# Performance work log

Hardware: AMD Instinct MI355X
Metric: run time of the kernel (lower is better)

The kernel has to match this reference:

```python
import jax, jax.numpy as jnp
import numpy as np

NUM_OBJ = 3
MIN_OBJ_SCALE = 0.1
MAX_OBJ_SCALE = 0.8
MIN_Y_SCALE = 0.75
MAX_Y_SCALE = 1.25
OBJ_POS_BOUND = 0.9
EPS_FIX = 0.095
BIG = 1e12


def setup_inputs() -> dict:
    key = jax.random.key(0)
    k1, k2, k3 = jax.random.split(key, 3)
    n, T, C, H, W = 64, 32, 3, 64, 64
    x = jax.random.normal(k1, (n, T, C, H, W), dtype=jnp.float32)
    d = C * H * W
    W_enc = jax.random.normal(k2, (d, NUM_OBJ * 8), dtype=jnp.float32) / np.sqrt(d).astype(np.float32)
    b_enc = jax.random.normal(k3, (NUM_OBJ * 8,), dtype=jnp.float32) * 0.01
    return {"x": x, "W_enc": W_enc, "b_enc": b_enc}


def _constrain_zp_mean(zp):
    # zp: (nTo, 8) -> mean (nTo, 4). std branch is discarded by forward().
    zm = jnp.concatenate([jax.nn.sigmoid(zp[:, 0:2]), 2.0 * jax.nn.sigmoid(zp[:, 2:4]) - 1.0], -1)
    set_max = jnp.array([[MAX_OBJ_SCALE - MIN_OBJ_SCALE, MAX_Y_SCALE - MIN_Y_SCALE, OBJ_POS_BOUND, OBJ_POS_BOUND]], dtype=zp.dtype)
    set_min = jnp.array([[MIN_OBJ_SCALE, MIN_Y_SCALE, 0.0, 0.0]], dtype=zp.dtype)
    return zm * set_max + set_min


def _greedy_assign(errors):
    # errors: (n, o, o). Greedy row-by-row argmin, masking out used columns with BIG,
    # exactly as the torch fault-fix loop does via scatter of 1e12.
    n, o, _ = errors.shape
    def step(used, i):
        e = errors[:, i, :] + used * BIG
        j = jnp.argmin(e, -1)
        used = used + jax.nn.one_hot(j, o, dtype=errors.dtype)
        return used, j
    _, js = jax.lax.scan(step, jnp.zeros((n, o), errors.dtype), jnp.arange(o))
    return jnp.moveaxis(js, 0, 1)  # (n, o)


def _match_objects(z):
    # z: (n, T, o, 4). Sequential greedy matching over time.
    def step(prev, z_t):
        curr = jax.lax.stop_gradient(z_t[:, :, 2:4])          # (n, o, 2)
        prv = jax.lax.stop_gradient(prev[:, :, 2:4])          # (n, o, 2)
        errors = jnp.sum((prv[:, :, None, :] - curr[:, None, :, :]) ** 2, -1)  # (n, i, j)
        idx = jnp.argmin(errors, -1)                          # (n, o)
        # fault = assignment is not a permutation (num_obj==3 check from source)
        ok = jnp.all(idx[:, 1:] != idx[:, :-1], -1) & (idx[:, 0] != idx[:, 2])
        gidx = _greedy_assign(errors)
        idx = jnp.where(ok[:, None], idx, gidx)
        match = jnp.take_along_axis(z_t, idx[:, :, None], axis=1)
        return match, match
    z0 = z[:, 0]
    _, rest = jax.lax.scan(step, z0, jnp.moveaxis(z[:, 1:], 1, 0))
    return jnp.concatenate([z0[:, None], jnp.moveaxis(rest, 0, 1)], 1)


def _fix_supair(z):
    # z: (n, T, o, 4). Replace isolated position jumps with neighbor average.
    n, T, o, d = z.shape
    diffs = jax.lax.stop_gradient(jnp.abs(z[:, 1:, :, :2] - z[:, :-1, :, :2]))
    zpad2 = jnp.zeros((n, 1, o, 2), z.dtype)
    prev = jnp.concatenate([zpad2, diffs], 1)
    after = jnp.concatenate([diffs, zpad2], 1)
    mask = (prev > EPS_FIX) & (after > EPS_FIX)               # (n, T, o, 2)
    zpad = jnp.zeros((n, 1, o, d), z.dtype)
    smooth = jnp.concatenate([zpad, (z[:, :-2] + z[:, 2:]) / 2, zpad], 1)
    mask_full = jnp.concatenate((d // 2) * [mask], -1)        # (n, T, o, 4)
    return jnp.where(mask_full, smooth, z)


def reference(x, W_enc, b_enc):
    n, T = x.shape[0], x.shape[1]
    # encoder: per-frame linear to (num_obj, 8) z-parameters
    zp = x.reshape(n * T, -1) @ W_enc + b_enc                  # (nT, o*8)
    zm = _constrain_zp_mean(zp.reshape(-1, 8))                 # (nTo, 4)
    z = zm.reshape(n, T, NUM_OBJ, 4)
    z = _match_objects(z)
    z = _fix_supair(z)
    # v_from_state
    v = z[:, 1:, :, 2:] - z[:, :-1, :, 2:]
    zf = jnp.concatenate([z[:, 1:], v], -1)                    # (n, T-1, o, 6)
    zf = jnp.concatenate([jnp.zeros_like(zf[:, 0:1]), zf], 1)  # (n, T, o, 6)
    zf = zf[:, 1:, :, 2:]                                      # (n, T-1, o, 4)
    zf = jnp.concatenate([(zf[..., :2] + 1) / 2 * 10, zf[..., 2:] / 2 * 10], -1)
    zf = jnp.concatenate([zf[..., :2] / 5, zf[..., 2:] * 2], -1)
    return zf
```

## Files before the change

### kernel.cpp

```cpp
#include <hip/hip_runtime.h>

#define N_B    64
#define T_S    32
#define DIM    12288
#define ROWS   2048
#define NCOL   12
#define KSPL   64
#define KSEG   (DIM / KSPL)
#define RPB    32
#define RPL    2

typedef float f4 __attribute__((ext_vector_type(4)));

#define ROR16_ADD(v, n)                                                        \
    v += __int_as_float(__builtin_amdgcn_update_dpp(                           \
        0, __float_as_int(v), 0x120 | (n), 0xF, 0xF, true))

__global__ __launch_bounds__(256, 5) void k_gemm3(const float* __restrict__ x,
                                                  const float* __restrict__ W,
                                                  float* __restrict__ part) {
    __shared__ float wt[NCOL * KSEG];
    const int tid  = threadIdx.x;
    const int w    = tid >> 6;
    const int lane = tid & 63;
    const int rg   = lane >> 4;
    const int kl   = lane & 15;
    const int rb   = blockIdx.x >> 6;
    const int sg   = blockIdx.x & 63;
    const int r0   = rb * RPB;
    const int k00  = sg * KSEG;

    float4 wv0 = make_float4(0.f, 0.f, 0.f, 0.f);
    float4 wv1 = wv0, wv2 = wv0;
    if (tid < KSEG) {
        const float* wr = W + (size_t)(k00 + tid) * 24;
        wv0 = *(const float4*)(wr + 0);
        wv1 = *(const float4*)(wr + 8);
        wv2 = *(const float4*)(wr + 16);
    }

    f4 xr[RPL][3];
#pragma unroll
    for (int r = 0; r < RPL; ++r) {
        const int row = r0 + w * 8 + rg * 2 + r;
        const float* xp = x + (size_t)row * DIM + k00 + kl * 4;
#pragma unroll
        for (int jj = 0; jj < 3; ++jj)
            xr[r][jj] = __builtin_nontemporal_load((const f4*)(xp + 64 * jj));
    }

    if (tid < KSEG) {
        wt[0 * KSEG + tid] = wv0.x;  wt[1 * KSEG + tid] = wv0.y;
        wt[2 * KSEG + tid] = wv0.z;  wt[3 * KSEG + tid] = wv0.w;
        wt[4 * KSEG + tid] = wv1.x;  wt[5 * KSEG + tid] = wv1.y;
        wt[6 * KSEG + tid] = wv1.z;  wt[7 * KSEG + tid] = wv1.w;
        wt[8 * KSEG + tid] = wv2.x;  wt[9 * KSEG + tid] = wv2.y;
        wt[10 * KSEG + tid] = wv2.z; wt[11 * KSEG + tid] = wv2.w;
    }
    __syncthreads();

    float acc[RPL][NCOL];
#pragma unroll
    for (int r = 0; r < RPL; ++r)
#pragma unroll
        for (int c = 0; c < NCOL; ++c) acc[r][c] = 0.f;

#pragma unroll
    for (int jj = 0; jj < 3; ++jj) {
        const int kq = kl * 4 + 64 * jj;
#pragma unroll
        for (int c = 0; c < NCOL; ++c) {
            const float4 q = *(const float4*)(wt + c * KSEG + kq);
#pragma unroll
            for (int r = 0; r < RPL; ++r)
                acc[r][c] += xr[r][jj].x * q.x + xr[r][jj].y * q.y +
                             xr[r][jj].z * q.z + xr[r][jj].w * q.w;
        }
    }

#pragma unroll
    for (int r = 0; r < RPL; ++r)
#pragma unroll
        for (int c = 0; c < NCOL; ++c) {
            float s = acc[r][c];
            ROR16_ADD(s, 1);
            ROR16_ADD(s, 2);
            ROR16_ADD(s, 4);
            ROR16_ADD(s, 8);
            acc[r][c] = s;
        }

    if (kl < NCOL) {
#pragma unroll
        for (int r = 0; r < RPL; ++r) {
            float v = acc[r][0];
#pragma unroll
            for (int c = 1; c < NCOL; ++c)
                if (kl == c) v = acc[r][c];
            const int row = r0 + w * 8 + rg * 2 + r;
            part[(size_t)sg * (ROWS * NCOL) + (size_t)row * NCOL + kl] = v;
        }
    }
}

__global__ __launch_bounds__(64) void k_post(const float* __restrict__ part,
                                             const float* __restrict__ b_enc,
                                             float* __restrict__ out) {
    __shared__ float z[T_S * NCOL];
    __shared__ float zm[T_S * NCOL];
    __shared__ float zf[T_S * NCOL];
    __shared__ int   perm[T_S];
    const int b   = blockIdx.x;
    const int tid = threadIdx.x;

#pragma unroll
    for (int ii = 0; ii < 6; ++ii) {
        const int i = tid + 64 * ii;
        float s = 0.f;
#pragma unroll 16
        for (int sgi = 0; sgi < KSPL; ++sgi)
            s += part[(size_t)sgi * (ROWS * NCOL) + b * 384 + i];
        const int c  = i % 12;
        const int o  = c >> 2;
        const int cp = c & 3;
        s += b_enc[o * 8 + cp];
        const float sgm = 1.f / (1.f + expf(-s));
        float v;
        if (cp == 0)      v = sgm * 0.7f + 0.1f;
        else if (cp == 1) v = sgm * 0.5f + 0.75f;
        else              v = (2.f * sgm - 1.f) * 0.9f;
        z[i] = v;
    }
    __syncthreads();

    if (tid == 0) {
        float px0 = z[2],  py0 = z[3];
        float px1 = z[6],  py1 = z[7];
        float px2 = z[10], py2 = z[11];
        for (int t = 1; t < T_S; ++t) {
            const int base = t * 12;
            const float cx0 = z[base + 2],  cy0 = z[base + 3];
            const float cx1 = z[base + 6],  cy1 = z[base + 7];
            const float cx2 = z[base + 10], cy2 = z[base + 11];

            float dx, dy;
            dx = px0 - cx0; dy = py0 - cy0; const float e00 = dx * dx + dy * dy;
            dx = px0 - cx1; dy = py0 - cy1; const float e01 = dx * dx + dy * dy;
            dx = px0 - cx2; dy = py0 - cy2; const float e02 = dx * dx + dy * dy;
            dx = px1 - cx0; dy = py1 - cy0; const float e10 = dx * dx + dy * dy;
            dx = px1 - cx1; dy = py1 - cy1; const float e11 = dx * dx + dy * dy;
            dx = px1 - cx2; dy = py1 - cy2; const float e12 = dx * dx + dy * dy;
            dx = px2 - cx0; dy = py2 - cy0; const float e20 = dx * dx + dy * dy;
            dx = px2 - cx1; dy = py2 - cy1; const float e21 = dx * dx + dy * dy;
            dx = px2 - cx2; dy = py2 - cy2; const float e22 = dx * dx + dy * dy;

            auto amin3 = [](float a0, float a1, float a2) {
                int j = 0; float e = a0;
                if (a1 < e) { e = a1; j = 1; }
                if (a2 < e) { j = 2; }
                return j;
            };
            int i0 = amin3(e00, e01, e02);
            int i1 = amin3(e10, e11, e12);
            int i2 = amin3(e20, e21, e22);
            const bool ok = (i1 != i0) && (i2 != i1) && (i0 != i2);
            if (!ok) {
                float u0 = 0.f, u1 = 0.f, u2 = 0.f;
                i0 = amin3(e00, e01, e02);
                if (i0 == 0) u0 = 1.f; else if (i0 == 1) u1 = 1.f; else u2 = 1.f;
                i1 = amin3(e10 + u0 * 1e12f, e11 + u1 * 1e12f, e12 + u2 * 1e12f);
                if (i1 == 0) u0 = 1.f; else if (i1 == 1) u1 = 1.f; else u2 = 1.f;
                i2 = amin3(e20 + u0 * 1e12f, e21 + u1 * 1e12f, e22 + u2 * 1e12f);
            }
            perm[t] = i0 * 9 + i1 * 3 + i2;
            px0 = (i0 == 0) ? cx0 : (i0 == 1) ? cx1 : cx2;
            py0 = (i0 == 0) ? cy0 : (i0 == 1) ? cy1 : cy2;
            px1 = (i1 == 0) ? cx0 : (i1 == 1) ? cx1 : cx2;
            py1 = (i1 == 0) ? cy0 : (i1 == 1) ? cy1 : cy2;
            px2 = (i2 == 0) ? cx0 : (i2 == 1) ? cx1 : cx2;
            py2 = (i2 == 0) ? cy0 : (i2 == 1) ? cy1 : cy2;
        }
    }
    __syncthreads();

#pragma unroll
    for (int ii = 0; ii < 6; ++ii) {
        const int i  = tid + 64 * ii;
        const int t  = i / 12;
        const int j  = i - t * 12;
        const int k  = j >> 2;
        const int ch = j & 3;
        int p = k;
        if (t > 0) {
            const int code = perm[t];
            p = (k == 0) ? code / 9 : (k == 1) ? (code % 9) / 3 : code % 3;
        }
        zm[i] = z[t * 12 + p * 4 + ch];
    }
    __syncthreads();

#pragma unroll
    for (int ii = 0; ii < 6; ++ii) {
        const int i  = tid + 64 * ii;
        const int t  = i / 12;
        const int j  = i - t * 12;
        const int o  = j >> 2;
        const int cc = j & 1;
        const int mb = o * 4 + cc;
        const float pd = (t >= 1)  ? fabsf(zm[t * 12 + mb] - zm[(t - 1) * 12 + mb]) : 0.f;
        const float ad = (t <= 30) ? fabsf(zm[(t + 1) * 12 + mb] - zm[t * 12 + mb]) : 0.f;
        const bool  m  = (pd > 0.095f) && (ad > 0.095f);
        const float sm = (t >= 1 && t <= 30)
                             ? (zm[(t - 1) * 12 + j] + zm[(t + 1) * 12 + j]) * 0.5f
                             : 0.f;
        zf[i] = m ? sm : zm[t * 12 + j];
    }
    __syncthreads();

    for (int i = tid; i < 31 * 12; i += 64) {
        const int t  = i / 12;
        const int j  = i - t * 12;
        const int o  = j >> 2;
        const int c2 = j & 3;
        const int pb = o * 4 + 2 + (c2 & 1);
        float v;
        if (c2 < 2) v = zf[(t + 1) * 12 + pb] + 1.f;
        else        v = (zf[(t + 1) * 12 + pb] - zf[t * 12 + pb]) * 10.f;
        out[b * 372 + i] = v;
    }
}

extern "C" void kernel_launch(void* const* d_in, const int* in_sizes, int n_in,
                              void* d_out, int out_size, void* d_ws, size_t ws_size,
                              hipStream_t stream) {
    (void)in_sizes; (void)n_in; (void)out_size; (void)ws_size;
    const float* x     = (const float*)d_in[0];
    const float* W_enc = (const float*)d_in[1];
    const float* b_enc = (const float*)d_in[2];
    float* out  = (float*)d_out;

    float* part = (float*)d_ws;

    k_gemm3<<<(ROWS / RPB) * KSPL, 256, 0, stream>>>(x, W_enc, part);
    k_post <<<N_B, 64, 0, stream>>>(part, b_enc, out);
}
```

Baseline: 171.6 us.

## Reduce split-K factor and double-buffer x loads across K sub-chunks

```diff
diff --git a/kernel.cpp b/kernel.cpp
--- a/kernel.cpp
+++ b/kernel.cpp
@@ -5,10 +5,11 @@
 #define DIM    12288
 #define ROWS   2048
 #define NCOL   12
-#define KSPL   64
+#define KSPL   8
 #define KSEG   (DIM / KSPL)
 #define RPB    32
 #define RPL    2
+#define NSUB   8
 
 typedef float f4 __attribute__((ext_vector_type(4)));
 
@@ -16,7 +17,7 @@
     v += __int_as_float(__builtin_amdgcn_update_dpp(                           \
         0, __float_as_int(v), 0x120 | (n), 0xF, 0xF, true))
 
-__global__ __launch_bounds__(256, 5) void k_gemm3(const float* __restrict__ x,
+__global__ __launch_bounds__(256, 2) void k_gemm4(const float* __restrict__ x,
                                                   const float* __restrict__ W,
                                                   float* __restrict__ part) {
     __shared__ float wt[NCOL * KSEG];
@@ -25,39 +26,29 @@
     const int lane = tid & 63;
     const int rg   = lane >> 4;
     const int kl   = lane & 15;
-    const int rb   = blockIdx.x >> 6;
-    const int sg   = blockIdx.x & 63;
+    const int rb   = blockIdx.x >> 3;
+    const int sg   = blockIdx.x & 7;
     const int r0   = rb * RPB;
     const int k00  = sg * KSEG;
 
-    float4 wv0 = make_float4(0.f, 0.f, 0.f, 0.f);
-    float4 wv1 = wv0, wv2 = wv0;
-    if (tid < KSEG) {
-        const float* wr = W + (size_t)(k00 + tid) * 24;
-        wv0 = *(const float4*)(wr + 0);
-        wv1 = *(const float4*)(wr + 8);
-        wv2 = *(const float4*)(wr + 16);
-    }
-
-    f4 xr[RPL][3];
-#pragma unroll
-    for (int r = 0; r < RPL; ++r) {
-        const int row = r0 + w * 8 + rg * 2 + r;
-        const float* xp = x + (size_t)row * DIM + k00 + kl * 4;
-#pragma unroll
-        for (int jj = 0; jj < 3; ++jj)
-            xr[r][jj] = __builtin_nontemporal_load((const f4*)(xp + 64 * jj));
-    }
-
-    if (tid < KSEG) {
-        wt[0 * KSEG + tid] = wv0.x;  wt[1 * KSEG + tid] = wv0.y;
-        wt[2 * KSEG + tid] = wv0.z;  wt[3 * KSEG + tid] = wv0.w;
-        wt[4 * KSEG + tid] = wv1.x;  wt[5 * KSEG + tid] = wv1.y;
-        wt[6 * KSEG + tid] = wv1.z;  wt[7 * KSEG + tid] = wv1.w;
-        wt[8 * KSEG + tid] = wv2.x;  wt[9 * KSEG + tid] = wv2.y;
-        wt[10 * KSEG + tid] = wv2.z; wt[11 * KSEG + tid] = wv2.w;
-    }
-    __syncthreads();
+#pragma unroll
+    for (int i = 0; i < 6; ++i) {
+        const int k = tid + 256 * i;
+        const float* wr = W + (size_t)(k00 + k) * 24;
+        const float4 a = *(const float4*)(wr + 0);
+        const float4 b = *(const float4*)(wr + 8);
+        const float4 c = *(const float4*)(wr + 16);
+        wt[0 * KSEG + k]  = a.x;  wt[1 * KSEG + k]  = a.y;
+        wt[2 * KSEG + k]  = a.z;  wt[3 * KSEG + k]  = a.w;
+        wt[4 * KSEG + k]  = b.x;  wt[5 * KSEG + k]  = b.y;
+        wt[6 * KSEG + k]  = b.z;  wt[7 * KSEG + k]  = b.w;
+        wt[8 * KSEG + k]  = c.x;  wt[9 * KSEG + k]  = c.y;
+        wt[10 * KSEG + k] = c.z;  wt[11 * KSEG + k] = c.w;
+    }
+    __syncthreads();
+
+    const float* xp0 = x + (size_t)(r0 + w * 8 + rg * 2 + 0) * DIM + k00 + kl * 4;
+    const float* xp1 = x + (size_t)(r0 + w * 8 + rg * 2 + 1) * DIM + k00 + kl * 4;
 
     float acc[RPL][NCOL];
 #pragma unroll
@@ -65,16 +56,37 @@
 #pragma unroll
         for (int c = 0; c < NCOL; ++c) acc[r][c] = 0.f;
 
-#pragma unroll
-    for (int jj = 0; jj < 3; ++jj) {
-        const int kq = kl * 4 + 64 * jj;
-#pragma unroll
-        for (int c = 0; c < NCOL; ++c) {
-            const float4 q = *(const float4*)(wt + c * KSEG + kq);
-#pragma unroll
-            for (int r = 0; r < RPL; ++r)
-                acc[r][c] += xr[r][jj].x * q.x + xr[r][jj].y * q.y +
-                             xr[r][jj].z * q.z + xr[r][jj].w * q.w;
+    f4 xb[2][RPL][3];
+#pragma unroll
+    for (int t = 0; t < 3; ++t) {
+        xb[0][0][t] = __builtin_nontemporal_load((const f4*)(xp0 + 64 * t));
+        xb[0][1][t] = __builtin_nontemporal_load((const f4*)(xp1 + 64 * t));
+    }
+
+#pragma unroll
+    for (int j = 0; j < NSUB; ++j) {
+        const int cur = j & 1, nxt = cur ^ 1;
+        if (j + 1 < NSUB) {
+            const int off = 192 * (j + 1);
+#pragma unroll
+            for (int t = 0; t < 3; ++t) {
+                xb[nxt][0][t] =
+                    __builtin_nontemporal_load((const f4*)(xp0 + off + 64 * t));
+                xb[nxt][1][t] =
+                    __builtin_nontemporal_load((const f4*)(xp1 + off + 64 * t));
+            }
+        }
+#pragma unroll
+        for (int t = 0; t < 3; ++t) {
+            const int kq = kl * 4 + 192 * j + 64 * t;
+#pragma unroll
+            for (int c = 0; c < NCOL; ++c) {
+                const float4 q = *(const float4*)(wt + c * KSEG + kq);
+#pragma unroll
+                for (int r = 0; r < RPL; ++r)
+                    acc[r][c] += xb[cur][r][t].x * q.x + xb[cur][r][t].y * q.y +
+                                 xb[cur][r][t].z * q.z + xb[cur][r][t].w * q.w;
+            }
         }
     }
 
@@ -117,7 +129,7 @@
     for (int ii = 0; ii < 6; ++ii) {
         const int i = tid + 64 * ii;
         float s = 0.f;
-#pragma unroll 16
+#pragma unroll
         for (int sgi = 0; sgi < KSPL; ++sgi)
             s += part[(size_t)sgi * (ROWS * NCOL) + b * 384 + i];
         const int c  = i % 12;
@@ -241,6 +253,6 @@
 
     float* part = (float*)d_ws;
 
-    k_gemm3<<<(ROWS / RPB) * KSPL, 256, 0, stream>>>(x, W_enc, part);
+    k_gemm4<<<(ROWS / RPB) * KSPL, 256, 0, stream>>>(x, W_enc, part);
     k_post <<<N_B, 64, 0, stream>>>(part, b_enc, out);
 }
```

Result: faster. 162.5 us (median of 2 runs) (-5.3%).
